# Optimization experiments

Measured on AMD Instinct MI355X. Metric: run time of the kernel, lower is better.

The kernel has to match this reference:

```python
import jax, jax.numpy as jnp
import numpy as np

N_NODES = 100000
N_EDGES = 1_600_000
D_FEAT = 64


def setup_inputs() -> dict:
    key = jax.random.key(0)
    kx, ke = jax.random.split(key)
    x = jax.random.normal(kx, (N_NODES, D_FEAT), dtype=jnp.float32)
    edge_index = jax.random.randint(ke, (2, N_EDGES), 0, N_NODES, dtype=jnp.int64)
    return {"x": x, "edge_index": edge_index}


def reference(x, edge_index):
    # GCN symmetric normalization without self loops, then SpMM aggregation.
    # adj[row, col] = 1; deg[i] = row-sum of adj; norm_e = d[row]^-1/2 * d[col]^-1/2
    n = x.shape[0]
    row, col = edge_index[0], edge_index[1]
    ones = jnp.ones(row.shape, dtype=x.dtype)
    deg = jax.ops.segment_sum(ones, row, num_segments=n)  # [N]
    dinv = jnp.where(deg > 0, jax.lax.rsqrt(jnp.maximum(deg, 1)), jnp.zeros_like(deg))
    norm = dinv[row] * dinv[col]  # [E] per-edge coefficient
    # gather-scale-scatter: out[i] = sum_{(i,j) in E} norm_ij * x[j]
    x_neighbors_norm = jax.ops.segment_sum(norm[:, None] * x[col], row, num_segments=n)
    return jnp.concatenate([x, x_neighbors_norm], axis=-1)  # [N, 2d]
```

## Files before the change

### kernel.cpp

```cpp
#include <hip/hip_runtime.h>

#define THREADS 256
#define EB 256
#define BSHIFT 7
#define BROWS (1 << BSHIFT)
#define MAXNB 1024

__global__ void bucket_hist(const int* __restrict__ row, int* __restrict__ h,
                            int E, int per, int NB) {
    __shared__ int lds[MAXNB];
    for (int k = threadIdx.x; k < NB; k += blockDim.x) lds[k] = 0;
    __syncthreads();
    int lo = blockIdx.x * per;
    int hi = min(E, lo + per);
    for (int i = lo + threadIdx.x; i < hi; i += blockDim.x)
        atomicAdd(&lds[row[i] >> BSHIFT], 1);
    __syncthreads();
    int* hb = h + (size_t)blockIdx.x * NB;
    for (int k = threadIdx.x; k < NB; k += blockDim.x) hb[k] = lds[k];
}

__global__ void scan_cols(int* __restrict__ h, int* __restrict__ totals, int NB) {
    int k = blockIdx.x;
    int lane = threadIdx.x;
    int carry = 0;
#pragma unroll
    for (int base = 0; base < EB; base += 64) {
        int idx = (base + lane) * NB + k;
        int v = h[idx];
        int s = v;
#pragma unroll
        for (int off = 1; off < 64; off <<= 1) {
            int t = __shfl_up(s, off, 64);
            if (lane >= off) s += t;
        }
        h[idx] = carry + s - v;
        carry += __shfl(s, 63, 64);
    }
    if (lane == 0) totals[k] = carry;
}

__global__ void scan_totals(const int* __restrict__ totals, int* __restrict__ bstart,
                            int* __restrict__ row_start, int NB, int N, int E) {
    int lane = threadIdx.x;
    int carry = 0;
    for (int base = 0; base < NB; base += 64) {
        int i = base + lane;
        int v = (i < NB) ? totals[i] : 0;
        int s = v;
#pragma unroll
        for (int off = 1; off < 64; off <<= 1) {
            int t = __shfl_up(s, off, 64);
            if (lane >= off) s += t;
        }
        if (i < NB) bstart[i] = carry + s - v;
        carry += __shfl(s, 63, 64);
    }
    if (lane == 0) { bstart[NB] = E; row_start[N] = E; }
}

__global__ void bucket_scatter(const int* __restrict__ row, const int* __restrict__ col,
                               const int* __restrict__ h, const int* __restrict__ bstart,
                               unsigned long long* __restrict__ sorted,
                               int E, int per, int NB) {
    __shared__ int cur[MAXNB];
    const int* hb = h + (size_t)blockIdx.x * NB;
    for (int k = threadIdx.x; k < NB; k += blockDim.x) cur[k] = bstart[k] + hb[k];
    __syncthreads();
    int lo = blockIdx.x * per;
    int hi = min(E, lo + per);
    for (int i = lo + threadIdx.x; i < hi; i += blockDim.x) {
        int r = row[i];
        int pos = atomicAdd(&cur[r >> BSHIFT], 1);
        sorted[pos] = ((unsigned long long)(unsigned)r << 32) | (unsigned)col[i];
    }
}

__global__ void bucket_group(const unsigned long long* __restrict__ sorted,
                             const int* __restrict__ bstart,
                             int* __restrict__ csr_col, int* __restrict__ row_start,
                             float* __restrict__ dinv, int N, int NB) {
    __shared__ int hist[BROWS];
    __shared__ int cur[BROWS];
    int k = blockIdx.x;
    int base = bstart[k];
    int cnt = bstart[k + 1] - base;
    for (int r = threadIdx.x; r < BROWS; r += blockDim.x) hist[r] = 0;
    __syncthreads();
    for (int i = threadIdx.x; i < cnt; i += blockDim.x) {
        int r = (int)(sorted[base + i] >> 32) & (BROWS - 1);
        atomicAdd(&hist[r], 1);
    }
    __syncthreads();
    if (threadIdx.x < 64) {
        int lane = threadIdx.x;
        int carry = 0;
#pragma unroll
        for (int b2 = 0; b2 < BROWS; b2 += 64) {
            int v = hist[b2 + lane];
            int s = v;
#pragma unroll
            for (int off = 1; off < 64; off <<= 1) {
                int t = __shfl_up(s, off, 64);
                if (lane >= off) s += t;
            }
            int pref = carry + s - v;
            cur[b2 + lane] = pref;
            int node = (k << BSHIFT) + b2 + lane;
            if (node < N) {
                row_start[node] = base + pref;
                dinv[node] = (v > 0) ? rsqrtf((float)v) : 0.f;
            }
            carry += __shfl(s, 63, 64);
        }
    }
    __syncthreads();
    for (int i = threadIdx.x; i < cnt; i += blockDim.x) {
        unsigned long long rc = sorted[base + i];
        int r = (int)(rc >> 32) & (BROWS - 1);
        int pos = base + atomicAdd(&cur[r], 1);
        csr_col[pos] = (int)(unsigned)rc;
    }
}

__device__ inline unsigned short bf16_rne(float f) {
    union { float f; unsigned u; } t; t.f = f;
    unsigned u = t.u;
    u += 0x7FFFu + ((u >> 16) & 1u);
    return (unsigned short)(u >> 16);
}

__global__ void scale_copy(const float4* __restrict__ x4, const float* __restrict__ dinv,
                           float4* __restrict__ out4, ushort4* __restrict__ y4, int total) {
    int i = blockIdx.x * blockDim.x + threadIdx.x;
    if (i >= total) return;
    int n = i >> 4, q = i & 15;
    float4 v = x4[i];
    float w = dinv[n];
    out4[(size_t)n * 32 + q] = v;
    ushort4 h;
    h.x = bf16_rne(v.x * w);
    h.y = bf16_rne(v.y * w);
    h.z = bf16_rne(v.z * w);
    h.w = bf16_rne(v.w * w);
    y4[i] = h;
}

__global__ void aggregate(const uint4* __restrict__ y16,
                          const int* __restrict__ row_start,
                          const int* __restrict__ csr_col,
                          const float* __restrict__ dinv,
                          float4* __restrict__ out4, int N) {
    int wid = threadIdx.x >> 6;
    int lane = threadIdx.x & 63;
    int g = lane >> 3;
    int q = lane & 7;
    int node = (blockIdx.x * (blockDim.x >> 6) + wid) * 8 + g;
    if (node >= N) return;

    int s = row_start[node];
    int e = row_start[node + 1];
    float a0 = 0.f, a1 = 0.f, a2 = 0.f, a3 = 0.f, a4 = 0.f, a5 = 0.f, a6 = 0.f, a7 = 0.f;
    int i = s;
    for (; i + 1 < e; i += 2) {
        int c0 = csr_col[i];
        int c1 = csr_col[i + 1];
        uint4 v0 = y16[(size_t)c0 * 8 + q];
        uint4 v1 = y16[(size_t)c1 * 8 + q];
        a0 += __uint_as_float(v0.x << 16);
        a1 += __uint_as_float(v0.x & 0xFFFF0000u);
        a2 += __uint_as_float(v0.y << 16);
        a3 += __uint_as_float(v0.y & 0xFFFF0000u);
        a4 += __uint_as_float(v0.z << 16);
        a5 += __uint_as_float(v0.z & 0xFFFF0000u);
        a6 += __uint_as_float(v0.w << 16);
        a7 += __uint_as_float(v0.w & 0xFFFF0000u);
        a0 += __uint_as_float(v1.x << 16);
        a1 += __uint_as_float(v1.x & 0xFFFF0000u);
        a2 += __uint_as_float(v1.y << 16);
        a3 += __uint_as_float(v1.y & 0xFFFF0000u);
        a4 += __uint_as_float(v1.z << 16);
        a5 += __uint_as_float(v1.z & 0xFFFF0000u);
        a6 += __uint_as_float(v1.w << 16);
        a7 += __uint_as_float(v1.w & 0xFFFF0000u);
    }
    if (i < e) {
        int c0 = csr_col[i];
        uint4 v0 = y16[(size_t)c0 * 8 + q];
        a0 += __uint_as_float(v0.x << 16);
        a1 += __uint_as_float(v0.x & 0xFFFF0000u);
        a2 += __uint_as_float(v0.y << 16);
        a3 += __uint_as_float(v0.y & 0xFFFF0000u);
        a4 += __uint_as_float(v0.z << 16);
        a5 += __uint_as_float(v0.z & 0xFFFF0000u);
        a6 += __uint_as_float(v0.w << 16);
        a7 += __uint_as_float(v0.w & 0xFFFF0000u);
    }
    float w0 = dinv[node];
    float4 r0 = make_float4(a0 * w0, a1 * w0, a2 * w0, a3 * w0);
    float4 r1 = make_float4(a4 * w0, a5 * w0, a6 * w0, a7 * w0);
    size_t obase = (size_t)node * 32 + 16 + q * 2;
    out4[obase] = r0;
    out4[obase + 1] = r1;
}

extern "C" void kernel_launch(void* const* d_in, const int* in_sizes, int n_in,
                              void* d_out, int out_size, void* d_ws, size_t ws_size,
                              hipStream_t stream) {
    const float* x = (const float*)d_in[0];
    const int* ei = (const int*)d_in[1];

    const int N = in_sizes[0] / 64;
    const int E = in_sizes[1] / 2;
    const int* row = ei;
    const int* col = ei + E;

    const int NB = (N + BROWS - 1) >> BSHIFT;
    const int per = (E + EB - 1) / EB;

    char* ws = (char*)d_ws;
    unsigned long long* sorted = (unsigned long long*)ws; ws += (size_t)E * 8;
    int* h         = (int*)ws;   ws += (size_t)EB * NB * sizeof(int);
    int* totals    = (int*)ws;   ws += (size_t)NB * sizeof(int);
    int* bstart    = (int*)ws;   ws += (size_t)(NB + 1) * sizeof(int);
    int* row_start = (int*)ws;   ws += (size_t)(N + 1) * sizeof(int);
    float* dinv    = (float*)ws; ws += (size_t)N * sizeof(float);
    int* csr_col   = (int*)ws;
    ushort4* y4 = (ushort4*)sorted;

    float* out = (float*)d_out;

    bucket_hist<<<EB, THREADS, 0, stream>>>(row, h, E, per, NB);
    scan_cols<<<NB, 64, 0, stream>>>(h, totals, NB);
    scan_totals<<<1, 64, 0, stream>>>(totals, bstart, row_start, NB, N, E);
    bucket_scatter<<<EB, THREADS, 0, stream>>>(row, col, h, bstart, sorted, E, per, NB);
    bucket_group<<<NB, THREADS, 0, stream>>>(sorted, bstart, csr_col, row_start, dinv, N, NB);

    int total = N * 16;
    scale_copy<<<(total + THREADS - 1) / THREADS, THREADS, 0, stream>>>(
        (const float4*)x, dinv, (float4*)out, y4, total);

    int nodes_per_block = (THREADS / 64) * 8;
    int blocks = (N + nodes_per_block - 1) / nodes_per_block;
    aggregate<<<blocks, THREADS, 0, stream>>>((const uint4*)y4, row_start, csr_col,
                                              dinv, (float4*)out, N);
}
```

Measured before the change: 104.6 us.

## Pack sorted edges into 32-bit keys, add nontemporal loads/stores, unroll aggregation by four

The intermediate sorted edge array now packs the local row offset (7 bits) and column (17 bits) into a 32-bit word instead of a 64-bit pair, halving scatter write and group read traffic. Nontemporal loads and stores are added for streaming accesses to edge indices, x, and output. The aggregation loop is unrolled to four gathers in flight. The packing assumes node ids fit in 17 bits, which holds for N=100000 but breaks for larger graphs.

```diff
diff --git a/kernel.cpp b/kernel.cpp
--- a/kernel.cpp
+++ b/kernel.cpp
@@ -5,6 +5,9 @@
 #define BSHIFT 7
 #define BROWS (1 << BSHIFT)
 #define MAXNB 1024
+#define COLBITS 17
+
+typedef float f32x4 __attribute__((ext_vector_type(4)));
 
 __global__ void bucket_hist(const int* __restrict__ row, int* __restrict__ h,
                             int E, int per, int NB) {
@@ -14,7 +17,7 @@
     int lo = blockIdx.x * per;
     int hi = min(E, lo + per);
     for (int i = lo + threadIdx.x; i < hi; i += blockDim.x)
-        atomicAdd(&lds[row[i] >> BSHIFT], 1);
+        atomicAdd(&lds[__builtin_nontemporal_load(row + i) >> BSHIFT], 1);
     __syncthreads();
     int* hb = h + (size_t)blockIdx.x * NB;
     for (int k = threadIdx.x; k < NB; k += blockDim.x) hb[k] = lds[k];
@@ -61,7 +64,7 @@
 
 __global__ void bucket_scatter(const int* __restrict__ row, const int* __restrict__ col,
                                const int* __restrict__ h, const int* __restrict__ bstart,
-                               unsigned long long* __restrict__ sorted,
+                               unsigned* __restrict__ sorted,
                                int E, int per, int NB) {
     __shared__ int cur[MAXNB];
     const int* hb = h + (size_t)blockIdx.x * NB;
@@ -70,16 +73,17 @@
     int lo = blockIdx.x * per;
     int hi = min(E, lo + per);
     for (int i = lo + threadIdx.x; i < hi; i += blockDim.x) {
-        int r = row[i];
+        int r = __builtin_nontemporal_load(row + i);
+        int c = __builtin_nontemporal_load(col + i);
         int pos = atomicAdd(&cur[r >> BSHIFT], 1);
-        sorted[pos] = ((unsigned long long)(unsigned)r << 32) | (unsigned)col[i];
-    }
-}
-
-__global__ void bucket_group(const unsigned long long* __restrict__ sorted,
+        sorted[pos] = ((unsigned)(r & (BROWS - 1)) << COLBITS) | (unsigned)c;
+    }
+}
+
+__global__ void bucket_group(const unsigned* __restrict__ sorted,
                              const int* __restrict__ bstart,
                              int* __restrict__ csr_col, int* __restrict__ row_start,
-                             float* __restrict__ dinv, int N, int NB) {
+                             float* __restrict__ dinv, int N) {
     __shared__ int hist[BROWS];
     __shared__ int cur[BROWS];
     int k = blockIdx.x;
@@ -87,10 +91,8 @@
     int cnt = bstart[k + 1] - base;
     for (int r = threadIdx.x; r < BROWS; r += blockDim.x) hist[r] = 0;
     __syncthreads();
-    for (int i = threadIdx.x; i < cnt; i += blockDim.x) {
-        int r = (int)(sorted[base + i] >> 32) & (BROWS - 1);
-        atomicAdd(&hist[r], 1);
-    }
+    for (int i = threadIdx.x; i < cnt; i += blockDim.x)
+        atomicAdd(&hist[sorted[base + i] >> COLBITS], 1);
     __syncthreads();
     if (threadIdx.x < 64) {
         int lane = threadIdx.x;
@@ -116,10 +118,10 @@
     }
     __syncthreads();
     for (int i = threadIdx.x; i < cnt; i += blockDim.x) {
-        unsigned long long rc = sorted[base + i];
-        int r = (int)(rc >> 32) & (BROWS - 1);
+        unsigned rc = sorted[base + i];
+        int r = (int)(rc >> COLBITS);
         int pos = base + atomicAdd(&cur[r], 1);
-        csr_col[pos] = (int)(unsigned)rc;
+        csr_col[pos] = (int)(rc & ((1u << COLBITS) - 1));
     }
 }
 
@@ -130,14 +132,14 @@
     return (unsigned short)(u >> 16);
 }
 
-__global__ void scale_copy(const float4* __restrict__ x4, const float* __restrict__ dinv,
-                           float4* __restrict__ out4, ushort4* __restrict__ y4, int total) {
+__global__ void scale_copy(const f32x4* __restrict__ x4, const float* __restrict__ dinv,
+                           f32x4* __restrict__ out4, ushort4* __restrict__ y4, int total) {
     int i = blockIdx.x * blockDim.x + threadIdx.x;
     if (i >= total) return;
     int n = i >> 4, q = i & 15;
-    float4 v = x4[i];
+    f32x4 v = __builtin_nontemporal_load(x4 + i);
     float w = dinv[n];
-    out4[(size_t)n * 32 + q] = v;
+    __builtin_nontemporal_store(v, out4 + (size_t)n * 32 + q);
     ushort4 h;
     h.x = bf16_rne(v.x * w);
     h.y = bf16_rne(v.y * w);
@@ -146,11 +148,22 @@
     y4[i] = h;
 }
 
+__device__ __forceinline__ void acc_bf16x8(float a[8], uint4 v) {
+    a[0] += __uint_as_float(v.x << 16);
+    a[1] += __uint_as_float(v.x & 0xFFFF0000u);
+    a[2] += __uint_as_float(v.y << 16);
+    a[3] += __uint_as_float(v.y & 0xFFFF0000u);
+    a[4] += __uint_as_float(v.z << 16);
+    a[5] += __uint_as_float(v.z & 0xFFFF0000u);
+    a[6] += __uint_as_float(v.w << 16);
+    a[7] += __uint_as_float(v.w & 0xFFFF0000u);
+}
+
 __global__ void aggregate(const uint4* __restrict__ y16,
                           const int* __restrict__ row_start,
                           const int* __restrict__ csr_col,
                           const float* __restrict__ dinv,
-                          float4* __restrict__ out4, int N) {
+                          f32x4* __restrict__ out4, int N) {
     int wid = threadIdx.x >> 6;
     int lane = threadIdx.x & 63;
     int g = lane >> 3;
@@ -160,48 +173,32 @@
 
     int s = row_start[node];
     int e = row_start[node + 1];
-    float a0 = 0.f, a1 = 0.f, a2 = 0.f, a3 = 0.f, a4 = 0.f, a5 = 0.f, a6 = 0.f, a7 = 0.f;
+    float a[8] = {0.f, 0.f, 0.f, 0.f, 0.f, 0.f, 0.f, 0.f};
     int i = s;
-    for (; i + 1 < e; i += 2) {
-        int c0 = csr_col[i];
-        int c1 = csr_col[i + 1];
+    for (; i + 3 < e; i += 4) {
+        int c0 = __builtin_nontemporal_load(csr_col + i);
+        int c1 = __builtin_nontemporal_load(csr_col + i + 1);
+        int c2 = __builtin_nontemporal_load(csr_col + i + 2);
+        int c3 = __builtin_nontemporal_load(csr_col + i + 3);
         uint4 v0 = y16[(size_t)c0 * 8 + q];
         uint4 v1 = y16[(size_t)c1 * 8 + q];
-        a0 += __uint_as_float(v0.x << 16);
-        a1 += __uint_as_float(v0.x & 0xFFFF0000u);
-        a2 += __uint_as_float(v0.y << 16);
-        a3 += __uint_as_float(v0.y & 0xFFFF0000u);
-        a4 += __uint_as_float(v0.z << 16);
-        a5 += __uint_as_float(v0.z & 0xFFFF0000u);
-        a6 += __uint_as_float(v0.w << 16);
-        a7 += __uint_as_float(v0.w & 0xFFFF0000u);
-        a0 += __uint_as_float(v1.x << 16);
-        a1 += __uint_as_float(v1.x & 0xFFFF0000u);
-        a2 += __uint_as_float(v1.y << 16);
-        a3 += __uint_as_float(v1.y & 0xFFFF0000u);
-        a4 += __uint_as_float(v1.z << 16);
-        a5 += __uint_as_float(v1.z & 0xFFFF0000u);
-        a6 += __uint_as_float(v1.w << 16);
-        a7 += __uint_as_float(v1.w & 0xFFFF0000u);
-    }
-    if (i < e) {
-        int c0 = csr_col[i];
-        uint4 v0 = y16[(size_t)c0 * 8 + q];
-        a0 += __uint_as_float(v0.x << 16);
-        a1 += __uint_as_float(v0.x & 0xFFFF0000u);
-        a2 += __uint_as_float(v0.y << 16);
-        a3 += __uint_as_float(v0.y & 0xFFFF0000u);
-        a4 += __uint_as_float(v0.z << 16);
-        a5 += __uint_as_float(v0.z & 0xFFFF0000u);
-        a6 += __uint_as_float(v0.w << 16);
-        a7 += __uint_as_float(v0.w & 0xFFFF0000u);
+        uint4 v2 = y16[(size_t)c2 * 8 + q];
+        uint4 v3 = y16[(size_t)c3 * 8 + q];
+        acc_bf16x8(a, v0);
+        acc_bf16x8(a, v1);
+        acc_bf16x8(a, v2);
+        acc_bf16x8(a, v3);
+    }
+    for (; i < e; ++i) {
+        int c = __builtin_nontemporal_load(csr_col + i);
+        acc_bf16x8(a, y16[(size_t)c * 8 + q]);
     }
     float w0 = dinv[node];
-    float4 r0 = make_float4(a0 * w0, a1 * w0, a2 * w0, a3 * w0);
-    float4 r1 = make_float4(a4 * w0, a5 * w0, a6 * w0, a7 * w0);
+    f32x4 r0 = {a[0] * w0, a[1] * w0, a[2] * w0, a[3] * w0};
+    f32x4 r1 = {a[4] * w0, a[5] * w0, a[6] * w0, a[7] * w0};
     size_t obase = (size_t)node * 32 + 16 + q * 2;
-    out4[obase] = r0;
-    out4[obase + 1] = r1;
+    __builtin_nontemporal_store(r0, out4 + obase);
+    __builtin_nontemporal_store(r1, out4 + obase + 1);
 }
 
 extern "C" void kernel_launch(void* const* d_in, const int* in_sizes, int n_in,
@@ -219,14 +216,16 @@
     const int per = (E + EB - 1) / EB;
 
     char* ws = (char*)d_ws;
-    unsigned long long* sorted = (unsigned long long*)ws; ws += (size_t)E * 8;
+    size_t slab0 = (size_t)N * 128;
+    if ((size_t)E * 4 > slab0) slab0 = (size_t)E * 4;
+    unsigned* sorted = (unsigned*)ws;
+    ushort4* y4      = (ushort4*)ws;  ws += slab0;
     int* h         = (int*)ws;   ws += (size_t)EB * NB * sizeof(int);
     int* totals    = (int*)ws;   ws += (size_t)NB * sizeof(int);
     int* bstart    = (int*)ws;   ws += (size_t)(NB + 1) * sizeof(int);
     int* row_start = (int*)ws;   ws += (size_t)(N + 1) * sizeof(int);
     float* dinv    = (float*)ws; ws += (size_t)N * sizeof(float);
     int* csr_col   = (int*)ws;
-    ushort4* y4 = (ushort4*)sorted;
 
     float* out = (float*)d_out;
 
@@ -234,14 +233,14 @@
     scan_cols<<<NB, 64, 0, stream>>>(h, totals, NB);
     scan_totals<<<1, 64, 0, stream>>>(totals, bstart, row_start, NB, N, E);
     bucket_scatter<<<EB, THREADS, 0, stream>>>(row, col, h, bstart, sorted, E, per, NB);
-    bucket_group<<<NB, THREADS, 0, stream>>>(sorted, bstart, csr_col, row_start, dinv, N, NB);
+    bucket_group<<<NB, THREADS, 0, stream>>>(sorted, bstart, csr_col, row_start, dinv, N);
 
     int total = N * 16;
     scale_copy<<<(total + THREADS - 1) / THREADS, THREADS, 0, stream>>>(
-        (const float4*)x, dinv, (float4*)out, y4, total);
+        (const f32x4*)x, dinv, (f32x4*)out, y4, total);
 
     int nodes_per_block = (THREADS / 64) * 8;
     int blocks = (N + nodes_per_block - 1) / nodes_per_block;
     aggregate<<<blocks, THREADS, 0, stream>>>((const uint4*)y4, row_start, csr_col,
-                                              dinv, (float4*)out, N);
-}
+                                              dinv, (f32x4*)out, N);
+}
```

New measurement: 124.0 us. 1.19x slower.
